# Kernel optimization log

Hardware: AMD Instinct MI355X
Metric: run time of the kernel (lower is better)

## Reference

```python
import jax, jax.numpy as jnp
import numpy as np

N_NODES = 50000
N_EDGES = 800000
N_GRAPHS = 64
HEADS = 4
IN_CH, HID_CH, OUT_CH = 128, 64, 32


def setup_inputs() -> dict:
    key = jax.random.key(0)
    ks = jax.random.split(key, 13)
    x = jax.random.normal(ks[0], (N_NODES, IN_CH), dtype=jnp.float32)
    edge_index = jax.random.randint(ks[1], (2, N_EDGES), 0, N_NODES, dtype=jnp.int64)
    tensor_batch = jnp.sort(jax.random.randint(ks[2], (N_NODES,), 0, N_GRAPHS, dtype=jnp.int64))
    s = 0.1
    return {
        "x": x,
        "edge_index": edge_index,
        "tensor_batch": tensor_batch,
        "W1": jax.random.normal(ks[3], (IN_CH, HEADS * HID_CH), dtype=jnp.float32) * s,
        "a_src1": jax.random.normal(ks[4], (HEADS, HID_CH), dtype=jnp.float32) * s,
        "a_dst1": jax.random.normal(ks[5], (HEADS, HID_CH), dtype=jnp.float32) * s,
        "b1": jnp.zeros((HEADS * HID_CH,), dtype=jnp.float32),
        "W2": jax.random.normal(ks[6], (HEADS * HID_CH, HEADS * OUT_CH), dtype=jnp.float32) * s,
        "a_src2": jax.random.normal(ks[7], (HEADS, OUT_CH), dtype=jnp.float32) * s,
        "a_dst2": jax.random.normal(ks[8], (HEADS, OUT_CH), dtype=jnp.float32) * s,
        "b2": jnp.zeros((HEADS * OUT_CH,), dtype=jnp.float32),
        "Wout": jax.random.normal(ks[9], (HEADS * OUT_CH, 2), dtype=jnp.float32) * s,
        "bout": jnp.zeros((2,), dtype=jnp.float32),
    }


def gat_conv(x, src, dst, W, a_src, a_dst, b, heads, ch):
    """PyG-style GATConv (eval mode, self-loops already appended)."""
    N = x.shape[0]
    h = (x @ W).reshape(N, heads, ch)            # [N,H,C] per-head projection
    s = jnp.sum(h * a_src, axis=-1)              # [N,H] source attention term
    d = jnp.sum(h * a_dst, axis=-1)              # [N,H] dest attention term
    e = jax.nn.leaky_relu(s[src] + d[dst], negative_slope=0.2)   # [E,H]
    # segment softmax over incoming edges of each destination node
    m = jax.ops.segment_max(e, dst, num_segments=N)              # [N,H]
    ex = jnp.exp(e - m[dst])
    denom = jax.ops.segment_sum(ex, dst, num_segments=N)         # [N,H]
    alpha = ex / (denom[dst] + 1e-16)                            # [E,H]
    out = jax.ops.segment_sum(h[src] * alpha[:, :, None], dst, num_segments=N)
    return out.reshape(N, heads * ch) + b


def reference(x, edge_index, tensor_batch, W1, a_src1, a_dst1, b1,
              W2, a_src2, a_dst2, b2, Wout, bout):
    N = x.shape[0]
    loop = jnp.arange(N, dtype=edge_index.dtype)
    src = jnp.concatenate([edge_index[0], loop])  # add self-loops (PyG default)
    dst = jnp.concatenate([edge_index[1], loop])
    h = jax.nn.relu(gat_conv(x, src, dst, W1, a_src1, a_dst1, b1, HEADS, HID_CH))
    h = jax.nn.relu(gat_conv(h, src, dst, W2, a_src2, a_dst2, b2, HEADS, OUT_CH))
    # global mean pool per graph
    sums = jax.ops.segment_sum(h, tensor_batch, num_segments=N_GRAPHS)
    counts = jax.ops.segment_sum(jnp.ones((N, 1), h.dtype), tensor_batch, num_segments=N_GRAPHS)
    pooled = sums / jnp.maximum(counts, 1.0)
    logits = pooled @ Wout + bout
    return jax.nn.softmax(logits, axis=-1)
```

## Files before the change

### kernel.cpp

```cpp
#include <hip/hip_runtime.h>
#include <hip/hip_bf16.h>

#define N_NODES 50000
#define N_EDGES 800000
#define N_GRAPHS 64
#define HEADS 4
#define IN_CH 128
#define HID 64
#define F1 256
#define OUT_CH 32
#define F2 128
#define POOL_SPLITS 16
#define SCAN_B 256
#define SCAN_NB ((N_NODES + SCAN_B - 1) / SCAN_B)
#define GEMM_GRID ((N_NODES + 63) / 64)
#define COUNT_GRID ((N_EDGES + 255) / 256)
#define SCATTER_GRID ((N_EDGES / 4 + 255) / 256)
#define AGEMM_GRID (N_NODES / 16)
#define HPAD 264

typedef unsigned short ushortT;
typedef unsigned int uintT;
typedef short v8s __attribute__((ext_vector_type(8)));
typedef float v4f __attribute__((ext_vector_type(4)));
typedef float v2f __attribute__((ext_vector_type(2)));

__device__ __forceinline__ ushortT f2bf(float f) {
    union { float f; unsigned int i; } v; v.f = f;
    unsigned int x = v.i;
    unsigned int r = (x + 0x7fffu + ((x >> 16) & 1u)) >> 16;
    return (ushortT)r;
}
__device__ __forceinline__ float bf_lo(uintT w) {
    union { unsigned int i; float f; } v; v.i = w << 16; return v.f;
}
__device__ __forceinline__ float bf_hi(uintT w) {
    union { unsigned int i; float f; } v; v.i = w & 0xffff0000u; return v.f;
}
__device__ __forceinline__ unsigned char f2fp8(float f) {
    return (unsigned char)__builtin_amdgcn_cvt_pk_fp8_f32(f, f, 0u, false);
}
__device__ __forceinline__ void fp8x4_acc(uintT w, float ex, float* acc) {
    v2f p0 = __builtin_amdgcn_cvt_pk_f32_fp8(w, false);
    v2f p1 = __builtin_amdgcn_cvt_pk_f32_fp8(w, true);
    acc[0] += ex * p0.x; acc[1] += ex * p0.y;
    acc[2] += ex * p1.x; acc[3] += ex * p1.y;
}

__device__ __forceinline__ void packW_one(const float* __restrict__ W,
                                          uint4* __restrict__ dst,
                                          int i, int FIN, int FOUT) {
    int KC = FIN / 32;
    int lane = i & 63, g = i >> 6;
    int kc = g % KC, nt = g / KC;
    int n = nt * 16 + (lane & 15);
    int kbase = kc * 32 + (lane >> 4) * 8;
    union { uint4 q; ushortT u[8]; } pk;
#pragma unroll
    for (int j = 0; j < 8; j++) pk.u[j] = f2bf(W[(kbase + j) * FOUT + n]);
    dst[i] = pk.q;
}

__global__ __launch_bounds__(256) void k_packw(
        const float* __restrict__ W1, const float* __restrict__ W2,
        uint4* __restrict__ wpk, int* __restrict__ counts) {
    int i = blockIdx.x * 256 + threadIdx.x;
    if (i < 4096) packW_one(W1, wpk, i, IN_CH, F1);
    else          packW_one(W2, wpk + 4096, i - 4096, F1, F2);
    for (int j = i; j < N_NODES; j += 8192) counts[j] = 0;
}

__device__ __forceinline__ void gemm1_body(const float* __restrict__ A,
                                           const uint4* __restrict__ Wpk,
                                           const float* __restrict__ ASrc,
                                           const float* __restrict__ ADst,
                                           unsigned char* __restrict__ out,
                                           float* __restrict__ s_out_g,
                                           float* __restrict__ d_out_g,
                                           int bid) {
    constexpr int KC = IN_CH / 32;
    constexpr int NT = F1 / 16;
    constexpr int NTH = (F1 / HEADS) / 16;
    int tid = threadIdx.x;
    int wave = tid >> 6, lane = tid & 63;
    long row0 = (long)bid * 64 + wave * 16;
    if (row0 >= N_NODES) return;
    int m = lane & 15, b = lane >> 4;

    v8s af[KC];
#pragma unroll
    for (int kc = 0; kc < KC; kc++) {
        union { v8s v; ushortT u[8]; } u;
        const float* p = A + (row0 + m) * IN_CH + kc * 32 + b * 8;
#pragma unroll
        for (int j = 0; j < 8; j++) u.u[j] = f2bf(p[j]);
        af[kc] = u.v;
    }

    float sp[4] = {0,0,0,0}, dp[4] = {0,0,0,0};
    float sk[4], dk[4];
#pragma unroll
    for (int nt = 0; nt < NT; nt++) {
        v4f c = {0.f, 0.f, 0.f, 0.f};
#pragma unroll
        for (int kc = 0; kc < KC; kc++) {
            union { v8s v; uint4 q; } bu;
            bu.q = Wpk[(nt * KC + kc) * 64 + lane];
            c = __builtin_amdgcn_mfma_f32_16x16x32_bf16(af[kc], bu.v, c, 0, 0, 0);
        }
        int col = nt * 16 + m;
        float av = ASrc[col], dv = ADst[col];
        long r0 = row0 + b * 4;
#pragma unroll
        for (int reg = 0; reg < 4; reg++) {
            out[(r0 + reg) * F1 + col] = f2fp8(c[reg]);
            sp[reg] += c[reg] * av;
            dp[reg] += c[reg] * dv;
        }
        if ((nt % NTH) == NTH - 1) {
#pragma unroll
            for (int o = 1; o < 16; o <<= 1) {
#pragma unroll
                for (int reg = 0; reg < 4; reg++) {
                    sp[reg] += __shfl_xor(sp[reg], o, 64);
                    dp[reg] += __shfl_xor(dp[reg], o, 64);
                }
            }
            int hd = nt / NTH;
#pragma unroll
            for (int reg = 0; reg < 4; reg++) {
                if (m == hd) { sk[reg] = sp[reg]; dk[reg] = dp[reg]; }
                sp[reg] = 0.f; dp[reg] = 0.f;
            }
        }
    }
    if (m < HEADS) {
        long r0 = row0 + b * 4;
#pragma unroll
        for (int reg = 0; reg < 4; reg++) {
            s_out_g[(r0 + reg) * HEADS + m] = sk[reg];
            d_out_g[(r0 + reg) * HEADS + m] = dk[reg];
        }
    }
}

__global__ __launch_bounds__(256) void k_mega1(
        const float* __restrict__ x, const uint4* __restrict__ wpk,
        const float* __restrict__ asrc1, const float* __restrict__ adst1,
        unsigned char* __restrict__ u_h, float* __restrict__ f_s,
        float* __restrict__ f_d, const int* __restrict__ ei,
        int* __restrict__ counts, int* __restrict__ rank) {
    if (blockIdx.x < GEMM_GRID) {
        gemm1_body(x, wpk, asrc1, adst1, u_h, f_s, f_d, blockIdx.x);
    } else {
        int e = (blockIdx.x - GEMM_GRID) * 256 + threadIdx.x;
        if (e < N_EDGES) {
            int dst = ei[N_EDGES + e];
            rank[e] = atomicAdd(&counts[dst], 1);
        }
    }
}

__global__ void k_scan1(const int* __restrict__ counts, int* __restrict__ offs,
                        int* __restrict__ bsum) {
    __shared__ int sh[SCAN_B];
    int b = blockIdx.x, t = threadIdx.x;
    int i = b * SCAN_B + t;
    int v = (i < N_NODES) ? counts[i] : 0;
    sh[t] = v;
    __syncthreads();
    for (int o = 1; o < SCAN_B; o <<= 1) {
        int add = (t >= o) ? sh[t - o] : 0;
        __syncthreads();
        sh[t] += add;
        __syncthreads();
    }
    if (i < N_NODES) offs[i] = sh[t] - v;
    if (t == SCAN_B - 1) bsum[b] = sh[t];
}

__global__ void k_scan2(const int* __restrict__ bsum, int* __restrict__ bbase,
                        int* __restrict__ offs, const int* __restrict__ batch,
                        int* __restrict__ bounds) {
    __shared__ int sh[SCAN_B];
    int t = threadIdx.x;
    int v = (t < SCAN_NB) ? bsum[t] : 0;
    sh[t] = v;
    __syncthreads();
    for (int o = 1; o < SCAN_B; o <<= 1) {
        int add = (t >= o) ? sh[t - o] : 0;
        __syncthreads();
        sh[t] += add;
        __syncthreads();
    }
    if (t < SCAN_NB) bbase[t] = sh[t] - v;
    if (t == SCAN_B - 1) offs[N_NODES] = sh[t];
    if (t <= N_GRAPHS) {
        int lo = 0, hi = N_NODES;
        while (lo < hi) {
            int mid = (lo + hi) >> 1;
            if (batch[mid] < t) lo = mid + 1; else hi = mid;
        }
        bounds[t] = lo;
    }
}

__global__ __launch_bounds__(256) void k_scatter(
        const int* __restrict__ ei, const int* __restrict__ offs,
        const int* __restrict__ bbase, const int* __restrict__ rank,
        int* __restrict__ csr_src) {
    int e4 = (blockIdx.x * 256 + threadIdx.x) * 4;
    if (e4 >= N_EDGES) return;
    int4 src = *(const int4*)(ei + e4);
    int4 dst = *(const int4*)(ei + N_EDGES + e4);
    int4 rk  = *(const int4*)(rank + e4);
    csr_src[offs[dst.x] + bbase[dst.x >> 8] + rk.x] = src.x;
    csr_src[offs[dst.y] + bbase[dst.y >> 8] + rk.y] = src.y;
    csr_src[offs[dst.z] + bbase[dst.z >> 8] + rk.z] = src.z;
    csr_src[offs[dst.w] + bbase[dst.w >> 8] + rk.w] = src.w;
}

__global__ __launch_bounds__(256) void k_aggemm(
        const unsigned char* __restrict__ hb, const float* __restrict__ s,
        const float* __restrict__ d, const int* __restrict__ offs,
        const int* __restrict__ bbase, const int* __restrict__ csr_src,
        const float* __restrict__ b1, const uint4* __restrict__ wpk2,
        const float* __restrict__ asrc2, const float* __restrict__ adst2,
        unsigned char* __restrict__ h2, float* __restrict__ s2,
        float* __restrict__ d2) {
    constexpr int CHUNK = 32;
    constexpr int TPN = 16;
    __shared__ int lsrc[4][4][CHUNK];
    __shared__ float lex[4][4][CHUNK * HEADS];
    __shared__ ushortT lh[16 * HPAD];
    int wv = threadIdx.x >> 6;
    int t = threadIdx.x & 63;
    int q = t >> 4, tl = t & 15;
    int nloc = wv * 4 + q;
    int n = blockIdx.x * 16 + nloc;
    int h = tl >> 2;
    int beg = offs[n] + bbase[n >> 8];
    int np1 = n + 1;
    int end = (np1 < N_NODES) ? offs[np1] + bbase[np1 >> 8] : offs[N_NODES];
    float4 dn = *(const float4*)(d + n * 4);

    float4 svn = *(const float4*)(s + n * 4);
    float ssel = (h == 0) ? svn.x : (h == 1) ? svn.y : (h == 2) ? svn.z : svn.w;
    float dsel = (h == 0) ? dn.x : (h == 1) ? dn.y : (h == 2) ? dn.z : dn.w;
    float es = ssel + dsel; es = es > 0.f ? es : 0.2f * es;
    float exs = __expf(es);
    float sumex = exs;
    float acc[16];
#pragma unroll
    for (int j = 0; j < 16; j++) acc[j] = 0.f;
    {
        uint4 w = ((const uint4*)hb)[(long)n * TPN + tl];
        fp8x4_acc(w.x, exs, acc);      fp8x4_acc(w.y, exs, acc + 4);
        fp8x4_acc(w.z, exs, acc + 8);  fp8x4_acc(w.w, exs, acc + 12);
    }

    int tot = end - beg;
    int m1 = max(tot, __shfl_xor(tot, 16, 64));
    int maxTot = max(m1, __shfl_xor(m1, 32, 64));
    for (int base = 0; base < maxTot; base += CHUNK) {
        int cnt = min(CHUNK, tot - base); if (cnt < 0) cnt = 0;
        int cntW = min(CHUNK, maxTot - base);
        for (int i = tl; i < cnt; i += TPN) {
            int sn = csr_src[beg + base + i];
            lsrc[wv][q][i] = sn;
            float4 sv = *(const float4*)(s + sn * 4);
            float e0 = sv.x + dn.x; e0 = e0 > 0.f ? e0 : 0.2f * e0;
            float e1 = sv.y + dn.y; e1 = e1 > 0.f ? e1 : 0.2f * e1;
            float e2 = sv.z + dn.z; e2 = e2 > 0.f ? e2 : 0.2f * e2;
            float e3 = sv.w + dn.w; e3 = e3 > 0.f ? e3 : 0.2f * e3;
            float4 exv = { __expf(e0), __expf(e1), __expf(e2), __expf(e3) };
            *(float4*)&lex[wv][q][i * 4] = exv;
        }
        asm volatile("s_waitcnt lgkmcnt(0)" ::: "memory");
#pragma unroll 4
        for (int i = 0; i < cntW; i++) {
            bool act = i < cnt;
            float ex = act ? lex[wv][q][i * 4 + h] : 0.f;
            int sn = act ? lsrc[wv][q][i] : 0;
            sumex += ex;
            uint4 w = ((const uint4*)hb)[(long)sn * TPN + tl];
            fp8x4_acc(w.x, ex, acc);      fp8x4_acc(w.y, ex, acc + 4);
            fp8x4_acc(w.z, ex, acc + 8);  fp8x4_acc(w.w, ex, acc + 12);
        }
        asm volatile("" ::: "memory");
    }
    float inv = 1.f / (sumex + 1e-16f);
    float o[16];
#pragma unroll
    for (int j = 0; j < 16; j++)
        o[j] = fmaxf(acc[j] * inv + b1[tl * 16 + j], 0.f);
    uint4 pk0, pk1;
    pk0.x = (uintT)f2bf(o[0])  | ((uintT)f2bf(o[1])  << 16);
    pk0.y = (uintT)f2bf(o[2])  | ((uintT)f2bf(o[3])  << 16);
    pk0.z = (uintT)f2bf(o[4])  | ((uintT)f2bf(o[5])  << 16);
    pk0.w = (uintT)f2bf(o[6])  | ((uintT)f2bf(o[7])  << 16);
    pk1.x = (uintT)f2bf(o[8])  | ((uintT)f2bf(o[9])  << 16);
    pk1.y = (uintT)f2bf(o[10]) | ((uintT)f2bf(o[11]) << 16);
    pk1.z = (uintT)f2bf(o[12]) | ((uintT)f2bf(o[13]) << 16);
    pk1.w = (uintT)f2bf(o[14]) | ((uintT)f2bf(o[15]) << 16);
    *(uint4*)&lh[nloc * HPAD + tl * 16]     = pk0;
    *(uint4*)&lh[nloc * HPAD + tl * 16 + 8] = pk1;
    __syncthreads();

    constexpr int KC = F1 / 32;
    constexpr int NTH2 = (F2 / HEADS) / 16;
    int wave = wv, lane = t;
    int m = lane & 15, b = lane >> 4;
    long row0 = (long)blockIdx.x * 16;

    v8s af[KC];
#pragma unroll
    for (int kc = 0; kc < KC; kc++) {
        union { v8s v; uint4 q; } u;
        u.q = *(const uint4*)&lh[m * HPAD + kc * 32 + b * 8];
        af[kc] = u.v;
    }

    float sp[4] = {0,0,0,0}, dp[4] = {0,0,0,0};
#pragma unroll
    for (int j = 0; j < NTH2; j++) {
        int nt = wave * NTH2 + j;
        v4f c = {0.f, 0.f, 0.f, 0.f};
#pragma unroll
        for (int kc = 0; kc < KC; kc++) {
            union { v8s v; uint4 q; } bu;
            bu.q = wpk2[(nt * KC + kc) * 64 + lane];
            c = __builtin_amdgcn_mfma_f32_16x16x32_bf16(af[kc], bu.v, c, 0, 0, 0);
        }
        int col = nt * 16 + m;
        float av = asrc2[col], dv = adst2[col];
#pragma unroll
        for (int reg = 0; reg < 4; reg++) {
            h2[(row0 + b * 4 + reg) * F2 + col] = f2fp8(c[reg]);
            sp[reg] += c[reg] * av;
            dp[reg] += c[reg] * dv;
        }
    }
#pragma unroll
    for (int o2 = 1; o2 < 16; o2 <<= 1) {
#pragma unroll
        for (int reg = 0; reg < 4; reg++) {
            sp[reg] += __shfl_xor(sp[reg], o2, 64);
            dp[reg] += __shfl_xor(dp[reg], o2, 64);
        }
    }
    if (m == 0) {
#pragma unroll
        for (int reg = 0; reg < 4; reg++) {
            s2[(row0 + b * 4 + reg) * HEADS + wave] = sp[reg];
            d2[(row0 + b * 4 + reg) * HEADS + wave] = dp[reg];
        }
    }
}

template <int C, int VEC, int WPB, int CHUNK>
__global__ __launch_bounds__(64 * WPB) void k_agg(
        const unsigned char* __restrict__ hb, const float* __restrict__ s,
        const float* __restrict__ d, const int* __restrict__ offs,
        const int* __restrict__ bbase, const int* __restrict__ csr_src,
        const float* __restrict__ bias, ushortT* __restrict__ xout) {
    constexpr int F = HEADS * C;
    constexpr int TPN = F / VEC;
    static_assert(TPN == 16, "four nodes per wave");
    static_assert(C / VEC == 4, "head = tl>>2");
    static_assert(N_NODES % (WPB * 4) == 0, "exact grid");
    __shared__ int lsrc[WPB][4][CHUNK];
    __shared__ float lex[WPB][4][CHUNK * HEADS];
    int wv = threadIdx.x >> 6;
    int t = threadIdx.x & 63;
    int q = t >> 4, tl = t & 15;
    int n = (blockIdx.x * WPB + wv) * 4 + q;
    int h = tl >> 2;
    int beg = offs[n] + bbase[n >> 8];
    int np1 = n + 1;
    int end = (np1 < N_NODES) ? offs[np1] + bbase[np1 >> 8] : offs[N_NODES];
    float4 dn = *(const float4*)(d + n * 4);

    float4 svn = *(const float4*)(s + n * 4);
    float ssel = (h == 0) ? svn.x : (h == 1) ? svn.y : (h == 2) ? svn.z : svn.w;
    float dsel = (h == 0) ? dn.x : (h == 1) ? dn.y : (h == 2) ? dn.z : dn.w;
    float es = ssel + dsel; es = es > 0.f ? es : 0.2f * es;
    float exs = __expf(es);
    float sumex = exs;
    float acc[VEC];
#pragma unroll
    for (int j = 0; j < VEC; j++) acc[j] = 0.f;
    {
        uint2 w = ((const uint2*)hb)[(long)n * TPN + tl];
        fp8x4_acc(w.x, exs, acc);      fp8x4_acc(w.y, exs, acc + 4);
    }

    int tot = end - beg;
    int m1 = max(tot, __shfl_xor(tot, 16, 64));
    int maxTot = max(m1, __shfl_xor(m1, 32, 64));
    for (int base = 0; base < maxTot; base += CHUNK) {
        int cnt = min(CHUNK, tot - base); if (cnt < 0) cnt = 0;
        int cntW = min(CHUNK, maxTot - base);
        for (int i = tl; i < cnt; i += TPN) {
            int sn = csr_src[beg + base + i];
            lsrc[wv][q][i] = sn;
            float4 sv = *(const float4*)(s + sn * 4);
            float e0 = sv.x + dn.x; e0 = e0 > 0.f ? e0 : 0.2f * e0;
            float e1 = sv.y + dn.y; e1 = e1 > 0.f ? e1 : 0.2f * e1;
            float e2 = sv.z + dn.z; e2 = e2 > 0.f ? e2 : 0.2f * e2;
            float e3 = sv.w + dn.w; e3 = e3 > 0.f ? e3 : 0.2f * e3;
            float4 exv = { __expf(e0), __expf(e1), __expf(e2), __expf(e3) };
            *(float4*)&lex[wv][q][i * 4] = exv;
        }
        asm volatile("s_waitcnt lgkmcnt(0)" ::: "memory");
#pragma unroll 4
        for (int i = 0; i < cntW; i++) {
            bool act = i < cnt;
            float ex = act ? lex[wv][q][i * 4 + h] : 0.f;
            int sn = act ? lsrc[wv][q][i] : 0;
            sumex += ex;
            uint2 w = ((const uint2*)hb)[(long)sn * TPN + tl];
            fp8x4_acc(w.x, ex, acc);      fp8x4_acc(w.y, ex, acc + 4);
        }
        asm volatile("" ::: "memory");
    }
    float inv = 1.f / (sumex + 1e-16f);
    float o[VEC];
#pragma unroll
    for (int j = 0; j < VEC; j++)
        o[j] = fmaxf(acc[j] * inv + bias[tl * VEC + j], 0.f);
    uint4 pk;
    pk.x = (uintT)f2bf(o[0]) | ((uintT)f2bf(o[1]) << 16);
    pk.y = (uintT)f2bf(o[2]) | ((uintT)f2bf(o[3]) << 16);
    pk.z = (uintT)f2bf(o[4]) | ((uintT)f2bf(o[5]) << 16);
    pk.w = (uintT)f2bf(o[6]) | ((uintT)f2bf(o[7]) << 16);
    ((uint4*)xout)[(long)n * TPN + tl] = pk;
}

__global__ void k_pool_partial(const ushortT* __restrict__ x2, const int* __restrict__ bounds,
                               float* __restrict__ partial) {
    int g = blockIdx.x, s = blockIdx.y;
    int t = threadIdx.x;
    int half = t >> 6, tl = t & 63;
    int n0 = bounds[g], n1 = bounds[g + 1];
    int len = n1 - n0;
    int a = n0 + (int)((long)len * s / POOL_SPLITS);
    int b = n0 + (int)((long)len * (s + 1) / POOL_SPLITS);
    float a0 = 0.f, a1 = 0.f;
    const uintT* x2u = (const uintT*)x2;
    for (int n = a + half; n < b; n += 2) {
        uintT w = x2u[(long)n * 64 + tl];
        a0 += bf_lo(w); a1 += bf_hi(w);
    }
    float2 pr = {a0, a1};
    *(float2*)&partial[(((long)g * 2 * POOL_SPLITS) + (s * 2 + half)) * F2 + 2 * tl] = pr;
}

__global__ void k_head(const float* __restrict__ partial, const int* __restrict__ bounds,
                       const float* __restrict__ Wout, const float* __restrict__ bout,
                       float* __restrict__ out) {
    __shared__ float red0[F2], red1[F2];
    int g = blockIdx.x;
    int t = threadIdx.x;
    int cntN = bounds[g + 1] - bounds[g];
    float cnt = fmaxf((float)cntN, 1.0f);
    float sum = 0.f;
    for (int s = 0; s < 2 * POOL_SPLITS; s++)
        sum += partial[((long)g * 2 * POOL_SPLITS + s) * F2 + t];
    float p = sum / cnt;
    red0[t] = p * Wout[t * 2 + 0];
    red1[t] = p * Wout[t * 2 + 1];
    __syncthreads();
    for (int off = F2 / 2; off > 0; off >>= 1) {
        if (t < off) { red0[t] += red0[t + off]; red1[t] += red1[t + off]; }
        __syncthreads();
    }
    if (t == 0) {
        float l0 = red0[0] + bout[0];
        float l1 = red1[0] + bout[1];
        float m = fmaxf(l0, l1);
        float e0 = __expf(l0 - m), e1 = __expf(l1 - m);
        float inv = 1.f / (e0 + e1);
        out[g * 2 + 0] = e0 * inv;
        out[g * 2 + 1] = e1 * inv;
    }
}

extern "C" void kernel_launch(void* const* d_in, const int* in_sizes, int n_in,
                              void* d_out, int out_size, void* d_ws, size_t ws_size,
                              hipStream_t stream) {
    const float* x     = (const float*)d_in[0];
    const int*   ei    = (const int*)d_in[1];
    const int*   batch = (const int*)d_in[2];
    const float* W1    = (const float*)d_in[3];
    const float* asrc1 = (const float*)d_in[4];
    const float* adst1 = (const float*)d_in[5];
    const float* b1    = (const float*)d_in[6];
    const float* W2    = (const float*)d_in[7];
    const float* asrc2 = (const float*)d_in[8];
    const float* adst2 = (const float*)d_in[9];
    const float* b2    = (const float*)d_in[10];
    const float* Wout  = (const float*)d_in[11];
    const float* bout  = (const float*)d_in[12];

    char* ws = (char*)d_ws;
    size_t off = 0;
    auto alloc = [&](size_t bytes) -> void* {
        void* p = ws + off;
        off += (bytes + 255) / 256 * 256;
        return p;
    };
    unsigned char* u_h = (unsigned char*)alloc((size_t)N_NODES * F1);
    unsigned char* u_h2 = (unsigned char*)alloc((size_t)N_NODES * F2);
    ushortT* u_x2  = (ushortT*)alloc(sizeof(ushortT) * (size_t)N_NODES * F2);
    uint4*   wpk   = (uint4*)alloc(sizeof(uint4) * 8192);
    float*   f_s   = (float*)alloc(sizeof(float) * (size_t)N_NODES * HEADS);
    float*   f_d   = (float*)alloc(sizeof(float) * (size_t)N_NODES * HEADS);
    float*   f_s2  = (float*)alloc(sizeof(float) * (size_t)N_NODES * HEADS);
    float*   f_d2  = (float*)alloc(sizeof(float) * (size_t)N_NODES * HEADS);
    int*     i_cnt = (int*)alloc(sizeof(int) * (size_t)N_NODES);
    int*     i_off = (int*)alloc(sizeof(int) * (size_t)(N_NODES + 1));
    int*     i_rnk = (int*)alloc(sizeof(int) * (size_t)N_EDGES);
    int*     i_csr = (int*)alloc(sizeof(int) * (size_t)N_EDGES);
    int*     i_bnd = (int*)alloc(sizeof(int) * (size_t)(N_GRAPHS + 1));
    int*     i_bs  = (int*)alloc(sizeof(int) * SCAN_NB);
    int*     i_bb  = (int*)alloc(sizeof(int) * SCAN_NB);
    float*   f_prt = (float*)alloc(sizeof(float) * (size_t)N_GRAPHS * 2 * POOL_SPLITS * F2);
    (void)ws_size; (void)in_sizes; (void)n_in; (void)out_size;

    k_packw<<<32, 256, 0, stream>>>(W1, W2, wpk, i_cnt);

    k_mega1<<<GEMM_GRID + COUNT_GRID, 256, 0, stream>>>(
        x, wpk, asrc1, adst1, u_h, f_s, f_d, ei, i_cnt, i_rnk);

    k_scan1<<<SCAN_NB, SCAN_B, 0, stream>>>(i_cnt, i_off, i_bs);
    k_scan2<<<1, SCAN_B, 0, stream>>>(i_bs, i_bb, i_off, batch, i_bnd);
    k_scatter<<<SCATTER_GRID, 256, 0, stream>>>(ei, i_off, i_bb, i_rnk, i_csr);

    k_aggemm<<<AGEMM_GRID, 256, 0, stream>>>(
        u_h, f_s, f_d, i_off, i_bb, i_csr, b1, wpk + 4096, asrc2, adst2,
        u_h2, f_s2, f_d2);

    int agg_grid = N_NODES / (4 * 4);
    k_agg<OUT_CH, 8, 4, 64><<<agg_grid, 256, 0, stream>>>(
        u_h2, f_s2, f_d2, i_off, i_bb, i_csr, b2, u_x2);

    dim3 pgrid(N_GRAPHS, POOL_SPLITS);
    k_pool_partial<<<pgrid, F2, 0, stream>>>(u_x2, i_bnd, f_prt);
    k_head<<<N_GRAPHS, F2, 0, stream>>>(f_prt, i_bnd, Wout, bout, (float*)d_out);
}
```

Measured before the change: 238.2 us.

## Fuse layer-2 aggregation with mean-pool partial sums, drop pool kernel

The second-layer GAT aggregation kernel now reduces its 16 output nodes per block in shared memory into per-graph partial sums, assuming each 16-node block spans at most two graphs because the batch vector is sorted. This removes the bf16 x2 intermediate write and read and the separate pool_partial launch. The head kernel sums the per-block partials covering each graph's node range. It also halves the CHUNK size, which adds an extra block barrier and an extra head-loop length that grows with graph size.

```diff
diff --git a/kernel.cpp b/kernel.cpp
--- a/kernel.cpp
+++ b/kernel.cpp
@@ -10,7 +10,6 @@
 #define F1 256
 #define OUT_CH 32
 #define F2 128
-#define POOL_SPLITS 16
 #define SCAN_B 256
 #define SCAN_NB ((N_NODES + SCAN_B - 1) / SCAN_B)
 #define GEMM_GRID ((N_NODES + 63) / 64)
@@ -33,9 +32,6 @@
 }
 __device__ __forceinline__ float bf_lo(uintT w) {
     union { unsigned int i; float f; } v; v.i = w << 16; return v.f;
-}
-__device__ __forceinline__ float bf_hi(uintT w) {
-    union { unsigned int i; float f; } v; v.i = w & 0xffff0000u; return v.f;
 }
 __device__ __forceinline__ unsigned char f2fp8(float f) {
     return (unsigned char)__builtin_amdgcn_cvt_pk_fp8_f32(f, f, 0u, false);
@@ -358,24 +354,27 @@
     }
 }
 
-template <int C, int VEC, int WPB, int CHUNK>
-__global__ __launch_bounds__(64 * WPB) void k_agg(
+__global__ __launch_bounds__(256) void k_agg2pool(
         const unsigned char* __restrict__ hb, const float* __restrict__ s,
         const float* __restrict__ d, const int* __restrict__ offs,
         const int* __restrict__ bbase, const int* __restrict__ csr_src,
-        const float* __restrict__ bias, ushortT* __restrict__ xout) {
-    constexpr int F = HEADS * C;
-    constexpr int TPN = F / VEC;
-    static_assert(TPN == 16, "four nodes per wave");
-    static_assert(C / VEC == 4, "head = tl>>2");
-    static_assert(N_NODES % (WPB * 4) == 0, "exact grid");
-    __shared__ int lsrc[WPB][4][CHUNK];
-    __shared__ float lex[WPB][4][CHUNK * HEADS];
+        const float* __restrict__ bias, const int* __restrict__ batch,
+        float* __restrict__ partial) {
+    constexpr int CHUNK = 32;
+    constexpr int TPN = 16;
+    constexpr int VEC = 8;
+    __shared__ int lsrc[4][4][CHUNK];
+    __shared__ float lex[4][4][CHUNK * HEADS];
+    __shared__ float lds_o[16][F2];
+    __shared__ int lgr[16];
     int wv = threadIdx.x >> 6;
     int t = threadIdx.x & 63;
     int q = t >> 4, tl = t & 15;
-    int n = (blockIdx.x * WPB + wv) * 4 + q;
+    int nloc = wv * 4 + q;
+    int n0blk = blockIdx.x * 16;
+    int n = n0blk + nloc;
     int h = tl >> 2;
+    if (threadIdx.x < 16) lgr[threadIdx.x] = batch[n0blk + threadIdx.x];
     int beg = offs[n] + bbase[n >> 8];
     int np1 = n + 1;
     int end = (np1 < N_NODES) ? offs[np1] + bbase[np1 >> 8] : offs[N_NODES];
@@ -425,48 +424,51 @@
         asm volatile("" ::: "memory");
     }
     float inv = 1.f / (sumex + 1e-16f);
-    float o[VEC];
-#pragma unroll
-    for (int j = 0; j < VEC; j++)
-        o[j] = fmaxf(acc[j] * inv + bias[tl * VEC + j], 0.f);
-    uint4 pk;
-    pk.x = (uintT)f2bf(o[0]) | ((uintT)f2bf(o[1]) << 16);
-    pk.y = (uintT)f2bf(o[2]) | ((uintT)f2bf(o[3]) << 16);
-    pk.z = (uintT)f2bf(o[4]) | ((uintT)f2bf(o[5]) << 16);
-    pk.w = (uintT)f2bf(o[6]) | ((uintT)f2bf(o[7]) << 16);
-    ((uint4*)xout)[(long)n * TPN + tl] = pk;
-}
-
-__global__ void k_pool_partial(const ushortT* __restrict__ x2, const int* __restrict__ bounds,
-                               float* __restrict__ partial) {
-    int g = blockIdx.x, s = blockIdx.y;
-    int t = threadIdx.x;
-    int half = t >> 6, tl = t & 63;
-    int n0 = bounds[g], n1 = bounds[g + 1];
-    int len = n1 - n0;
-    int a = n0 + (int)((long)len * s / POOL_SPLITS);
-    int b = n0 + (int)((long)len * (s + 1) / POOL_SPLITS);
-    float a0 = 0.f, a1 = 0.f;
-    const uintT* x2u = (const uintT*)x2;
-    for (int n = a + half; n < b; n += 2) {
-        uintT w = x2u[(long)n * 64 + tl];
-        a0 += bf_lo(w); a1 += bf_hi(w);
-    }
-    float2 pr = {a0, a1};
-    *(float2*)&partial[(((long)g * 2 * POOL_SPLITS) + (s * 2 + half)) * F2 + 2 * tl] = pr;
+    float4 o0, o1;
+    o0.x = fmaxf(acc[0] * inv + bias[tl * VEC + 0], 0.f);
+    o0.y = fmaxf(acc[1] * inv + bias[tl * VEC + 1], 0.f);
+    o0.z = fmaxf(acc[2] * inv + bias[tl * VEC + 2], 0.f);
+    o0.w = fmaxf(acc[3] * inv + bias[tl * VEC + 3], 0.f);
+    o1.x = fmaxf(acc[4] * inv + bias[tl * VEC + 4], 0.f);
+    o1.y = fmaxf(acc[5] * inv + bias[tl * VEC + 5], 0.f);
+    o1.z = fmaxf(acc[6] * inv + bias[tl * VEC + 6], 0.f);
+    o1.w = fmaxf(acc[7] * inv + bias[tl * VEC + 7], 0.f);
+    *(float4*)&lds_o[nloc][tl * VEC]     = o0;
+    *(float4*)&lds_o[nloc][tl * VEC + 4] = o1;
+    __syncthreads();
+
+    int tc = threadIdx.x;
+    if (tc < F2) {
+        int g0 = lgr[0];
+        float s0 = 0.f, s1 = 0.f;
+#pragma unroll
+        for (int r = 0; r < 16; r++) {
+            float v = lds_o[r][tc];
+            if (lgr[r] == g0) s0 += v; else s1 += v;
+        }
+        partial[((long)blockIdx.x * 2 + 0) * F2 + tc] = s0;
+        partial[((long)blockIdx.x * 2 + 1) * F2 + tc] = s1;
+    }
 }
 
 __global__ void k_head(const float* __restrict__ partial, const int* __restrict__ bounds,
+                       const int* __restrict__ batch,
                        const float* __restrict__ Wout, const float* __restrict__ bout,
                        float* __restrict__ out) {
     __shared__ float red0[F2], red1[F2];
     int g = blockIdx.x;
     int t = threadIdx.x;
-    int cntN = bounds[g + 1] - bounds[g];
-    float cnt = fmaxf((float)cntN, 1.0f);
+    int lo = bounds[g], hi = bounds[g + 1];
+    int len = hi - lo;
+    float cnt = fmaxf((float)len, 1.0f);
     float sum = 0.f;
-    for (int s = 0; s < 2 * POOL_SPLITS; s++)
-        sum += partial[((long)g * 2 * POOL_SPLITS + s) * F2 + t];
+    if (len > 0) {
+        int b0 = lo >> 4, b1 = (hi - 1) >> 4;
+        for (int b = b0; b <= b1; b++) {
+            int row = (batch[b * 16] == g) ? 0 : 1;
+            sum += partial[((long)b * 2 + row) * F2 + t];
+        }
+    }
     float p = sum / cnt;
     red0[t] = p * Wout[t * 2 + 0];
     red1[t] = p * Wout[t * 2 + 1];
@@ -512,7 +514,6 @@
     };
     unsigned char* u_h = (unsigned char*)alloc((size_t)N_NODES * F1);
     unsigned char* u_h2 = (unsigned char*)alloc((size_t)N_NODES * F2);
-    ushortT* u_x2  = (ushortT*)alloc(sizeof(ushortT) * (size_t)N_NODES * F2);
     uint4*   wpk   = (uint4*)alloc(sizeof(uint4) * 8192);
     float*   f_s   = (float*)alloc(sizeof(float) * (size_t)N_NODES * HEADS);
     float*   f_d   = (float*)alloc(sizeof(float) * (size_t)N_NODES * HEADS);
@@ -525,7 +526,7 @@
     int*     i_bnd = (int*)alloc(sizeof(int) * (size_t)(N_GRAPHS + 1));
     int*     i_bs  = (int*)alloc(sizeof(int) * SCAN_NB);
     int*     i_bb  = (int*)alloc(sizeof(int) * SCAN_NB);
-    float*   f_prt = (float*)alloc(sizeof(float) * (size_t)N_GRAPHS * 2 * POOL_SPLITS * F2);
+    float*   f_prt = (float*)alloc(sizeof(float) * (size_t)AGEMM_GRID * 2 * F2);
     (void)ws_size; (void)in_sizes; (void)n_in; (void)out_size;
 
     k_packw<<<32, 256, 0, stream>>>(W1, W2, wpk, i_cnt);
@@ -541,11 +542,9 @@
         u_h, f_s, f_d, i_off, i_bb, i_csr, b1, wpk + 4096, asrc2, adst2,
         u_h2, f_s2, f_d2);
 
-    int agg_grid = N_NODES / (4 * 4);
-    k_agg<OUT_CH, 8, 4, 64><<<agg_grid, 256, 0, stream>>>(
-        u_h2, f_s2, f_d2, i_off, i_bb, i_csr, b2, u_x2);
-
-    dim3 pgrid(N_GRAPHS, POOL_SPLITS);
-    k_pool_partial<<<pgrid, F2, 0, stream>>>(u_x2, i_bnd, f_prt);
-    k_head<<<N_GRAPHS, F2, 0, stream>>>(f_prt, i_bnd, Wout, bout, (float*)d_out);
-}
+    k_agg2pool<<<AGEMM_GRID, 256, 0, stream>>>(
+        u_h2, f_s2, f_d2, i_off, i_bb, i_csr, b2, batch, f_prt);
+
+    k_head<<<N_GRAPHS, F2, 0, stream>>>(f_prt, i_bnd, batch, Wout, bout,
+                                        (float*)d_out);
+}
```

Result: slower. 255.9 us (+7.4%).
